# Kernel optimization log

Hardware: AMD Instinct MI355X
Metric: run time of the kernel (lower is better)

The kernel has to match this reference:

```python
import jax, jax.numpy as jnp
import numpy as np
import math

B, S, H, E, TOPK, NHEADS = 8, 512, 1024, 8, 2, 8
CAP = int(B * S * 1.5 * TOPK / E)  # 1536


def _linear(x, w, b):
    # torch nn.Linear convention: y = x @ w.T + b, w: [out, in]
    return x @ w.T + b


def _mha(x, in_w, in_b, out_w, out_b, n_heads):
    # torch nn.MultiheadAttention self-attention, eval mode (no dropout)
    Bx, Sx, D = x.shape
    dh = D // n_heads
    qkv = x @ in_w.T + in_b                      # [B,S,3D]
    q, k, v = jnp.split(qkv, 3, axis=-1)
    def heads(t):
        return t.reshape(Bx, Sx, n_heads, dh).transpose(0, 2, 1, 3)  # [B,h,S,dh]
    q, k, v = heads(q), heads(k), heads(v)
    scores = jnp.einsum('bhqd,bhkd->bhqk', q, k) / math.sqrt(dh)
    attn = jax.nn.softmax(scores, axis=-1)
    o = jnp.einsum('bhqk,bhkd->bhqd', attn, v)   # [B,h,S,dh]
    o = o.transpose(0, 2, 1, 3).reshape(Bx, Sx, D)
    return o @ out_w.T + out_b


def setup_inputs() -> dict:
    key = jax.random.key(0)
    ks = jax.random.split(key, 24)
    sc = 0.02
    d = {
        'hidden_states': jax.random.normal(ks[0], (B, S, H), jnp.float32),
        'pos_emb': jax.random.normal(ks[1], (S, H), jnp.float32) * sc,
        'se_w1': jax.random.normal(ks[2], (H // 4, 1), jnp.float32) * sc,
        'se_b1': jnp.zeros((H // 4,), jnp.float32),
        'se_w2': jax.random.normal(ks[3], (H // 4, H // 4), jnp.float32) * sc,
        'se_b2': jnp.zeros((H // 4,), jnp.float32),
        'sexp_w': jax.random.normal(ks[4], (H, H // 4), jnp.float32) * sc,
        'sexp_b': jnp.zeros((H,), jnp.float32),
        'te_w1': jax.random.normal(ks[5], (H, H + 2), jnp.float32) * sc,
        'te_b1': jnp.zeros((H,), jnp.float32),
        'te_w2': jax.random.normal(ks[6], (H, H), jnp.float32) * sc,
        'te_b2': jnp.zeros((H,), jnp.float32),
        'attn_in_w': jax.random.normal(ks[7], (3 * H, H), jnp.float32) * sc,
        'attn_in_b': jnp.zeros((3 * H,), jnp.float32),
        'attn_out_w': jax.random.normal(ks[8], (H, H), jnp.float32) * sc,
        'attn_out_b': jnp.zeros((H,), jnp.float32),
        'tr_w1': jax.random.normal(ks[9], (H, H), jnp.float32) * sc,
        'tr_b1': jnp.zeros((H,), jnp.float32),
        'tr_w2': jax.random.normal(ks[10], (E, H), jnp.float32) * sc,
        'tr_b2': jnp.zeros((E,), jnp.float32),
    }
    return d


def reference(hidden_states, pos_emb, se_w1, se_b1, se_w2, se_b2, sexp_w, sexp_b,
              te_w1, te_b1, te_w2, te_b2, attn_in_w, attn_in_b, attn_out_w, attn_out_b,
              tr_w1, tr_b1, tr_w2, tr_b2):
    b, s, h = hidden_states.shape
    timestamps = jnp.arange(s, dtype=hidden_states.dtype)           # [S]
    seasonality = jnp.sin(timestamps * 2 * jnp.pi / 24)             # [S]
    ts_b = jnp.broadcast_to(timestamps, (b, s))
    se_b = jnp.broadcast_to(seasonality, (b, s))

    position_embeddings = pos_emb[:s][None]                          # [1,S,H]
    seas = jax.nn.relu(_linear(se_b[..., None], se_w1, se_b1))       # [B,S,H/4]
    seas = _linear(seas, se_w2, se_b2)
    seasonal_embeddings = _linear(seas, sexp_w, sexp_b)              # [B,S,H]

    time_features = jnp.stack([ts_b, se_b], axis=-1)                 # [B,S,2]
    combined = jnp.concatenate([hidden_states, time_features], -1)   # [B,S,H+2]
    enc = jax.nn.relu(_linear(combined, te_w1, te_b1))
    enc = _linear(enc, te_w2, te_b2)
    enc = enc + position_embeddings + seasonal_embeddings
    enc = _mha(enc, attn_in_w, attn_in_b, attn_out_w, attn_out_b, NHEADS)

    logits = _linear(jax.nn.relu(_linear(enc, tr_w1, tr_b1)), tr_w2, tr_b2)  # [B,S,E]
    router_probs = jax.nn.softmax(logits, axis=-1)
    top_k_probs, top_k_idx = jax.lax.top_k(router_probs, TOPK)
    top_k_probs = top_k_probs / top_k_probs.sum(-1, keepdims=True)

    capacity = int(b * s * 1.5 * TOPK / E)
    # top-k indices are distinct per token, so summed one-hots replicate the
    # python loop's slot-0 writes exactly.
    onehot = jax.nn.one_hot(top_k_idx, E, dtype=router_probs.dtype)  # [B,S,K,E]
    disp0 = onehot.sum(axis=2)                                        # [B,S,E]
    comb0 = jnp.einsum('bske,bsk->bse', onehot, top_k_probs)          # [B,S,E]
    dispatch = jnp.zeros((b, s, E, capacity), router_probs.dtype).at[:, :, :, 0].set(disp0)
    combine = jnp.zeros((b, s, E, capacity), router_probs.dtype).at[:, :, :, 0].set(comb0)

    p_mean = router_probs.mean(axis=(0, 1))
    aux_loss = jnp.sum(p_mean * jnp.log(p_mean * E + 1e-9))
    return dispatch, combine, router_probs, aux_loss
```

## Files before the change

kernel.cpp:

```cpp
#include <hip/hip_runtime.h>
#include <hip/hip_bf16.h>


#define Hh 1024

typedef __attribute__((ext_vector_type(8))) short short8v;
typedef __attribute__((ext_vector_type(4))) float f32x4;

static __device__ __forceinline__ ushort f2bf(float x) {
  uint u = __float_as_uint(x);
  u += 0x7FFF + ((u >> 16) & 1);
  return (ushort)(u >> 16);
}
static __device__ __forceinline__ float bf2f(ushort h) {
  return __uint_as_float(((uint)h) << 16);
}

template<int EPI, bool RELU, bool HAS_BN, bool HAS_BSN>
__global__ __launch_bounds__(256) void mgemm_k(
    const ushort* __restrict__ A, int lda, long long sAmaj, long long sAmin, int aHi, int aLo,
    const ushort* __restrict__ B, int ldb, long long sBmaj, long long sBmin, int bHi, int bLo,
    float* __restrict__ Cf, ushort* __restrict__ Ch, int ldc, long long sCmaj, long long sCmin,
    int splitOff, int Kd, int zdiv,
    const float* __restrict__ bN, const float* __restrict__ bSN, int ldbs, int smod,
    float alpha)
{
  int gx = gridDim.x, gy = gridDim.y;
  int lin = (blockIdx.z * gy + blockIdx.y) * gx + blockIdx.x;
  int nwg = gx * gy * gridDim.z;
  int cpx = nwg >> 3;
  int swz = (lin & 7) * cpx + (lin >> 3);
  int bz = swz / (gx * gy);
  int rem = swz - bz * (gx * gy);
  int by = rem / gx, bx = rem - by * gx;

  int zj = bz / zdiv, zi = bz - zj * zdiv;
  A += (size_t)zj * sAmaj + (size_t)zi * sAmin;
  B += (size_t)zj * sBmaj + (size_t)zi * sBmin;
  long long coff = (long long)zj * sCmaj + (long long)zi * sCmin;

  int m0 = by * 128, n0 = bx * 128;

  __shared__ __align__(16) ushort smem[32768];

  int t = threadIdx.x;
  int l = t & 63, w = t >> 6;
  int wm = w >> 1, wn = w & 1;

  f32x4 acc[4][4];
#pragma unroll
  for (int i = 0; i < 4; ++i)
#pragma unroll
    for (int j = 0; j < 4; ++j) acc[i][j] = (f32x4){0.f, 0.f, 0.f, 0.f};

  int srow = t >> 1;
  int sc = (t & 1) * 2;
  const ushort* gAh = A + (size_t)(m0 + srow) * lda + aHi + sc * 8;
  const ushort* gAl = A + (size_t)(m0 + srow) * lda + aLo + sc * 8;
  const ushort* gBh = B + (size_t)(n0 + srow) * ldb + bHi + sc * 8;
  const ushort* gBl = B + (size_t)(n0 + srow) * ldb + bLo + sc * 8;
  int wsw = ((srow >> 1) & 7) << 4;
  int wo0 = (srow * 64 + sc * 16) ^ wsw;
  int wo1 = (srow * 64 + sc * 16 + 16) ^ wsw;

  int aoff[4], boff[4];
#pragma unroll
  for (int mi = 0; mi < 4; ++mi) {
    int row = wm * 64 + mi * 16 + (l & 15);
    aoff[mi] = (row * 64 + (l >> 4) * 16) ^ (((row >> 1) & 7) << 4);
  }
#pragma unroll
  for (int ni = 0; ni < 4; ++ni) {
    int row = wn * 64 + ni * 16 + (l & 15);
    boff[ni] = (row * 64 + (l >> 4) * 16) ^ (((row >> 1) & 7) << 4);
  }

  int4 rAh0, rAh1, rAl0, rAl1, rBh0, rBh1, rBl0, rBl1;
#define LOADK(kc) do { \
    rAh0 = *(const int4*)(gAh + (kc));  rAh1 = *(const int4*)(gAh + (kc) + 8); \
    rAl0 = *(const int4*)(gAl + (kc));  rAl1 = *(const int4*)(gAl + (kc) + 8); \
    rBh0 = *(const int4*)(gBh + (kc));  rBh1 = *(const int4*)(gBh + (kc) + 8); \
    rBl0 = *(const int4*)(gBl + (kc));  rBl1 = *(const int4*)(gBl + (kc) + 8); \
  } while (0)
#define STOREK(bufbase) do { \
    char* nb_ = (char*)smem + (bufbase); \
    *(int4*)(nb_ + wo0) = rAh0;          *(int4*)(nb_ + wo1) = rAh1; \
    *(int4*)(nb_ + 8192 + wo0) = rAl0;   *(int4*)(nb_ + 8192 + wo1) = rAl1; \
    *(int4*)(nb_ + 16384 + wo0) = rBh0;  *(int4*)(nb_ + 16384 + wo1) = rBh1; \
    *(int4*)(nb_ + 24576 + wo0) = rBl0;  *(int4*)(nb_ + 24576 + wo1) = rBl1; \
  } while (0)

  int nt = Kd >> 5;
  LOADK(0);
  STOREK(0);
  __syncthreads();
  int cur = 0;
  for (int s2 = 0; s2 < nt; ++s2) {
    bool more = (s2 + 1 < nt);
    if (more) LOADK((s2 + 1) * 32);
    char* base = (char*)smem + cur * 32768;
    short8v ah[4], al[4], bb[4];
#pragma unroll
    for (int mi = 0; mi < 4; ++mi) ah[mi] = *(const short8v*)(base + aoff[mi]);
#pragma unroll
    for (int mi = 0; mi < 4; ++mi) al[mi] = *(const short8v*)(base + 8192 + aoff[mi]);
#pragma unroll
    for (int ni = 0; ni < 4; ++ni) bb[ni] = *(const short8v*)(base + 16384 + boff[ni]);
#pragma unroll
    for (int mi = 0; mi < 4; ++mi)
#pragma unroll
      for (int ni = 0; ni < 4; ++ni)
        acc[mi][ni] = __builtin_amdgcn_mfma_f32_16x16x32_bf16(ah[mi], bb[ni], acc[mi][ni], 0, 0, 0);
#pragma unroll
    for (int mi = 0; mi < 4; ++mi)
#pragma unroll
      for (int ni = 0; ni < 4; ++ni)
        acc[mi][ni] = __builtin_amdgcn_mfma_f32_16x16x32_bf16(al[mi], bb[ni], acc[mi][ni], 0, 0, 0);
#pragma unroll
    for (int ni = 0; ni < 4; ++ni) bb[ni] = *(const short8v*)(base + 24576 + boff[ni]);
#pragma unroll
    for (int mi = 0; mi < 4; ++mi)
#pragma unroll
      for (int ni = 0; ni < 4; ++ni)
        acc[mi][ni] = __builtin_amdgcn_mfma_f32_16x16x32_bf16(ah[mi], bb[ni], acc[mi][ni], 0, 0, 0);
    if (more) STOREK((cur ^ 1) * 32768);
    __syncthreads();
    cur ^= 1;
  }
#undef LOADK
#undef STOREK

#pragma unroll
  for (int mi = 0; mi < 4; ++mi)
#pragma unroll
    for (int j = 0; j < 4; ++j) {
      int m = m0 + wm * 64 + mi * 16 + (l >> 4) * 4 + j;
#pragma unroll
      for (int ni = 0; ni < 4; ++ni) {
        int n = n0 + wn * 64 + ni * 16 + (l & 15);
        float x = acc[mi][ni][j] * alpha;
        if (HAS_BN) x += bN[n];
        if (HAS_BSN) x += bSN[(size_t)(m % smod) * ldbs + n];
        if (RELU) x = fmaxf(x, 0.f);
        acc[mi][ni][j] = x;
      }
    }

  if (EPI == 0) {
    float* Fs = (float*)smem;
#pragma unroll
    for (int p = 0; p < 2; ++p) {
      __syncthreads();
      if (wm == p) {
#pragma unroll
        for (int mi = 0; mi < 4; ++mi)
#pragma unroll
          for (int j = 0; j < 4; ++j) {
            int r = mi * 16 + (l >> 4) * 4 + j;
#pragma unroll
            for (int ni = 0; ni < 4; ++ni) {
              int c = wn * 64 + ni * 16 + (l & 15);
              *(float*)((char*)Fs + ((r * 512 + c * 4) ^ ((r & 7) << 4))) = acc[mi][ni][j];
            }
          }
      }
      __syncthreads();
#pragma unroll
      for (int r8 = 0; r8 < 8; ++r8) {
        int idx = r8 * 256 + t;
        int row = idx >> 5, slot = idx & 31;
        int4 v = *(const int4*)((char*)Fs + ((row * 512 + slot * 16) ^ ((row & 7) << 4)));
        *(int4*)(Cf + coff + (size_t)(m0 + p * 64 + row) * ldc + n0 + slot * 4) = v;
      }
    }
  } else {
    __syncthreads();
    ushort* Es = smem;
#pragma unroll
    for (int pass = 0; pass < 2; ++pass) {
#pragma unroll
      for (int mi = 0; mi < 4; ++mi)
#pragma unroll
        for (int j = 0; j < 4; ++j) {
          int lr = wm * 64 + mi * 16 + (l >> 4) * 4 + j;
#pragma unroll
          for (int ni = 0; ni < 4; ++ni) {
            int lcb = (wn * 64 + ni * 16 + (l & 15)) * 2;
            float x = acc[mi][ni][j];
            ushort h = f2bf(x);
            ushort vv = (pass == 0) ? h : f2bf(x - bf2f(h));
            *(ushort*)((char*)Es + ((lr * 256 + lcb) ^ ((lr & 7) << 4))) = vv;
          }
        }
      __syncthreads();
      int off = (pass == 0) ? 0 : splitOff;
#pragma unroll
      for (int r = 0; r < 8; ++r) {
        int idx = r * 256 + t;
        int row = idx >> 4, cb = (idx & 15) * 16;
        int4 v = *(const int4*)((char*)Es + ((row * 256 + cb) ^ ((row & 7) << 4)));
        *(int4*)((char*)(Ch + coff + (size_t)(m0 + row) * ldc + off + n0) + cb) = v;
      }
      if (pass == 0) __syncthreads();
    }
  }
}

__global__ __launch_bounds__(256) void vtrans_k(
    const ushort* __restrict__ qkv2, ushort* __restrict__ Vt)
{
  int kt = blockIdx.x;
  int bh = blockIdx.y;
  int b = bh >> 3, h = bh & 7;
  __shared__ ushort VT[16384];
  int t = threadIdx.x;
#pragma unroll
  for (int seg = 0; seg < 2; ++seg) {
    int csrc = 2048 + h * 128 + seg * 3072;
    if (seg) __syncthreads();
#pragma unroll
    for (int r = 0; r < 8; ++r) {
      int idx = r * 256 + t;
      int k = idx >> 4, ds = idx & 15;
      int4 v = *(const int4*)(qkv2 + (size_t)(b * 512 + kt * 128 + k) * 6144 + csrc + ds * 8);
      ushort tmp[8];
      *(int4*)tmp = v;
#pragma unroll
      for (int j = 0; j < 8; ++j) {
        int d = ds * 8 + j;
        VT[d * 128 + (k ^ ((d >> 3) << 3))] = tmp[j];
      }
    }
    __syncthreads();
#pragma unroll
    for (int r = 0; r < 8; ++r) {
      int idx = r * 256 + t;
      int d = idx >> 4, os = idx & 15;
      int slot = os ^ (d >> 3);
      int4 v = *(const int4*)(VT + d * 128 + slot * 8);
      *(int4*)(Vt + (size_t)bh * 131072 + (size_t)d * 1024 + seg * 512 + kt * 128 + os * 8) = v;
    }
  }
}

__global__ __launch_bounds__(256) void convert_k(
    const float* __restrict__ W, int lda, ushort* __restrict__ Whl, int K)
{
  int r = blockIdx.x;
  int c = threadIdx.x * 4;
  const float* src = W + (size_t)r * lda + c;
  float x0 = src[0], x1 = src[1], x2 = src[2], x3 = src[3];
  ushort4 h, lo;
  h.x = f2bf(x0); lo.x = f2bf(x0 - bf2f(h.x));
  h.y = f2bf(x1); lo.y = f2bf(x1 - bf2f(h.y));
  h.z = f2bf(x2); lo.z = f2bf(x2 - bf2f(h.z));
  h.w = f2bf(x3); lo.w = f2bf(x3 - bf2f(h.w));
  ushort* dst = Whl + (size_t)r * 2 * K;
  *(ushort4*)&dst[c] = h;
  *(ushort4*)&dst[K + c] = lo;
}

__global__ __launch_bounds__(256) void precompute_k(
    const float* __restrict__ pos_emb,
    const float* __restrict__ se_w1, const float* __restrict__ se_b1,
    const float* __restrict__ se_w2, const float* __restrict__ se_b2,
    const float* __restrict__ sexp_w, const float* __restrict__ sexp_b,
    const float* __restrict__ te_w1, const float* __restrict__ te_b1,
    float* __restrict__ psea, float* __restrict__ bias1)
{
  int s = blockIdx.x, t = threadIdx.x;
  float ts = (float)s;
  float se = sinf(((ts * 2.0f) * 3.14159274101257324f) / 24.0f);
  __shared__ float l1[256], l2[256];
  l1[t] = fmaxf(se * se_w1[t] + se_b1[t], 0.f);
  __syncthreads();
  {
    float a = se_b2[t];
    const float* wr = se_w2 + (size_t)t * 256;
    for (int i = 0; i < 256; ++i) a += l1[i] * wr[i];
    l2[t] = a;
  }
  __syncthreads();
#pragma unroll
  for (int r = 0; r < 4; ++r) {
    int h = r * 256 + t;
    float v = sexp_b[h];
    const float* wr = sexp_w + (size_t)h * 256;
    for (int j = 0; j < 256; ++j) v += l2[j] * wr[j];
    psea[s * Hh + h] = pos_emb[s * Hh + h] + v;
    bias1[s * Hh + h] = te_b1[h] + ts * te_w1[(size_t)h * 1026 + 1024]
                                 + se * te_w1[(size_t)h * 1026 + 1025];
  }
}

__global__ __launch_bounds__(256) void softmax2_k(float* __restrict__ S)
{
  int row = blockIdx.x * 4 + (threadIdx.x >> 6);
  int lane = threadIdx.x & 63;
  float* p = S + (size_t)row * 512;
  float4 a = *(float4*)&p[lane * 4];
  float4 b = *(float4*)&p[256 + lane * 4];
  float m = fmaxf(fmaxf(fmaxf(a.x, a.y), fmaxf(a.z, a.w)),
                  fmaxf(fmaxf(b.x, b.y), fmaxf(b.z, b.w)));
#pragma unroll
  for (int off = 32; off; off >>= 1) m = fmaxf(m, __shfl_xor(m, off));
  a.x = expf(a.x - m); a.y = expf(a.y - m); a.z = expf(a.z - m); a.w = expf(a.w - m);
  b.x = expf(b.x - m); b.y = expf(b.y - m); b.z = expf(b.z - m); b.w = expf(b.w - m);
  float s = a.x + a.y + a.z + a.w + b.x + b.y + b.z + b.w;
#pragma unroll
  for (int off = 32; off; off >>= 1) s += __shfl_xor(s, off);
  float inv = 1.f / s;
  a.x *= inv; a.y *= inv; a.z *= inv; a.w *= inv;
  b.x *= inv; b.y *= inv; b.z *= inv; b.w *= inv;
  ushort* u = (ushort*)S + (size_t)row * 1024;
  ushort4 ha, la, hb, lb;
  ha.x = f2bf(a.x); la.x = f2bf(a.x - bf2f(ha.x));
  ha.y = f2bf(a.y); la.y = f2bf(a.y - bf2f(ha.y));
  ha.z = f2bf(a.z); la.z = f2bf(a.z - bf2f(ha.z));
  ha.w = f2bf(a.w); la.w = f2bf(a.w - bf2f(ha.w));
  hb.x = f2bf(b.x); lb.x = f2bf(b.x - bf2f(hb.x));
  hb.y = f2bf(b.y); lb.y = f2bf(b.y - bf2f(hb.y));
  hb.z = f2bf(b.z); lb.z = f2bf(b.z - bf2f(hb.z));
  hb.w = f2bf(b.w); lb.w = f2bf(b.w - bf2f(hb.w));
  *(ushort4*)&u[lane * 4] = ha;
  *(ushort4*)&u[512 + lane * 4] = la;
  *(ushort4*)&u[256 + lane * 4] = hb;
  *(ushort4*)&u[768 + lane * 4] = lb;
}

__global__ __launch_bounds__(256) void tr2_k(
    const float* __restrict__ h1, const float* __restrict__ w,
    const float* __restrict__ bias, float* __restrict__ logits)
{
  int wid = threadIdx.x >> 6, lane = threadIdx.x & 63;
  int t = blockIdx.x * 4 + wid;
  const float* x = h1 + (size_t)t * Hh;
  float acc[8];
#pragma unroll
  for (int e = 0; e < 8; ++e) acc[e] = 0.f;
  for (int k = lane; k < Hh; k += 64) {
    float xv = x[k];
#pragma unroll
    for (int e = 0; e < 8; ++e) acc[e] += xv * w[e * Hh + k];
  }
#pragma unroll
  for (int e = 0; e < 8; ++e) {
#pragma unroll
    for (int off = 32; off; off >>= 1) acc[e] += __shfl_xor(acc[e], off);
  }
  if (lane == 0) {
#pragma unroll
    for (int e = 0; e < 8; ++e) logits[(size_t)t * 8 + e] = acc[e] + bias[e];
  }
}

__global__ __launch_bounds__(256) void fill0_k(float4* __restrict__ p, long long n4)
{
  long long i = (long long)blockIdx.x * 256 + threadIdx.x;
  long long stride = (long long)gridDim.x * 256;
  float4 z = make_float4(0.f, 0.f, 0.f, 0.f);
  for (; i < n4; i += stride) p[i] = z;
}

__global__ __launch_bounds__(256) void router_k(
    float* __restrict__ out, float* __restrict__ partials)
{
  int t = blockIdx.x * 256 + threadIdx.x;
  float* lg = out + 100663296 + (size_t)t * 8;
  float p[8];
#pragma unroll
  for (int e = 0; e < 8; ++e) p[e] = lg[e];
  float m = p[0];
#pragma unroll
  for (int e = 1; e < 8; ++e) m = fmaxf(m, p[e]);
  float s = 0.f;
#pragma unroll
  for (int e = 0; e < 8; ++e) { p[e] = expf(p[e] - m); s += p[e]; }
  float inv = 1.f / s;
#pragma unroll
  for (int e = 0; e < 8; ++e) p[e] *= inv;
#pragma unroll
  for (int e = 0; e < 8; ++e) lg[e] = p[e];

  int i0 = 0; float v0 = p[0];
#pragma unroll
  for (int e = 1; e < 8; ++e) if (p[e] > v0) { v0 = p[e]; i0 = e; }
  int i1 = -1; float v1 = -1.f;
#pragma unroll
  for (int e = 0; e < 8; ++e) if (e != i0 && p[e] > v1) { v1 = p[e]; i1 = e; }
  float wn = 1.f / (v0 + v1);
  size_t db = (size_t)t * (8 * 1536);
  out[db + (size_t)i0 * 1536] = 1.f;
  out[db + (size_t)i1 * 1536] = 1.f;
  out[50331648 + db + (size_t)i0 * 1536] = v0 * wn;
  out[50331648 + db + (size_t)i1 * 1536] = v1 * wn;

  __shared__ float red[256];
#pragma unroll
  for (int e = 0; e < 8; ++e) {
    red[threadIdx.x] = p[e];
    __syncthreads();
    for (int st = 128; st; st >>= 1) {
      if (threadIdx.x < st) red[threadIdx.x] += red[threadIdx.x + st];
      __syncthreads();
    }
    if (threadIdx.x == 0) partials[blockIdx.x * 8 + e] = red[0];
    __syncthreads();
  }
}

__global__ __launch_bounds__(64) void aux_k(float* __restrict__ partials,
                                            float* __restrict__ out)
{
  int lane = threadIdx.x;
  float v = 0.f;
  if (lane < 8) {
    float s = 0.f;
    for (int b = 0; b < 16; ++b) s += partials[b * 8 + lane];
    float pm = s / 4096.f;
    v = pm * logf(pm * 8.f + 1e-9f);
  }
#pragma unroll
  for (int off = 4; off; off >>= 1) v += __shfl_xor(v, off);
  if (lane == 0) out[100696064] = v;
  partials[lane] = 0.f;
  partials[64 + lane] = 0.f;
}

extern "C" void kernel_launch(void* const* d_in, const int* in_sizes, int n_in,
                              void* d_out, int out_size, void* d_ws, size_t ws_size,
                              hipStream_t stream)
{
  const float* hidden = (const float*)d_in[0];
  const float* pos_emb = (const float*)d_in[1];
  const float* se_w1 = (const float*)d_in[2];
  const float* se_b1 = (const float*)d_in[3];
  const float* se_w2 = (const float*)d_in[4];
  const float* se_b2 = (const float*)d_in[5];
  const float* sexp_w = (const float*)d_in[6];
  const float* sexp_b = (const float*)d_in[7];
  const float* te_w1 = (const float*)d_in[8];
  const float* te_b1 = (const float*)d_in[9];
  const float* te_w2 = (const float*)d_in[10];
  const float* te_b2 = (const float*)d_in[11];
  const float* ain_w = (const float*)d_in[12];
  const float* ain_b = (const float*)d_in[13];
  const float* aout_w = (const float*)d_in[14];
  const float* aout_b = (const float*)d_in[15];
  const float* tr_w1 = (const float*)d_in[16];
  const float* tr_b1 = (const float*)d_in[17];
  const float* tr_w2 = (const float*)d_in[18];
  const float* tr_b2 = (const float*)d_in[19];
  float* out = (float*)d_out;

  char* arena = (char*)d_out;
  ushort* W1    = (ushort*)(arena + 0);
  ushort* W2h   = (ushort*)(arena + 4194304);
  ushort* Wa    = (ushort*)(arena + 8388608);
  ushort* Wo    = (ushort*)(arena + 20971520);
  ushort* Wt    = (ushort*)(arena + 25165824);
  ushort* hid2  = (ushort*)(arena + 29360128);
  ushort* enc1  = (ushort*)(arena + 46137344);
  ushort* enc2  = (ushort*)(arena + 62914560);
  ushort* qkv2  = (ushort*)(arena + 79691776);
  float*  scor  = (float*)(arena + 130023424);
  ushort* attno = (ushort*)(arena + 197132288);
  ushort* encf  = (ushort*)(arena + 213909504);
  float*  h1    = (float*)(arena + 230686720);
  float*  psea  = (float*)(arena + 247463936);
  float*  bias1 = (float*)(arena + 249561088);
  ushort* Vt    = (ushort*)(arena + 251658240);
  float*  parts = out + 51380224;
  float*  lgts  = out + 100663296;

  convert_k<<<1024, 256, 0, stream>>>(te_w1, 1026, W1, 1024);
  convert_k<<<1024, 256, 0, stream>>>(te_w2, 1024, W2h, 1024);
  convert_k<<<3072, 256, 0, stream>>>(ain_w, 1024, Wa, 1024);
  convert_k<<<1024, 256, 0, stream>>>(aout_w, 1024, Wo, 1024);
  convert_k<<<1024, 256, 0, stream>>>(tr_w1, 1024, Wt, 1024);
  convert_k<<<4096, 256, 0, stream>>>(hidden, 1024, hid2, 1024);

  precompute_k<<<512, 256, 0, stream>>>(pos_emb, se_w1, se_b1, se_w2, se_b2,
                                        sexp_w, sexp_b, te_w1, te_b1, psea, bias1);

  mgemm_k<1, true, false, true><<<dim3(8, 32, 1), 256, 0, stream>>>(
      hid2, 2048, 0, 0, 0, 1024,
      W1, 2048, 0, 0, 0, 1024,
      nullptr, enc1, 2048, 0, 0, 1024,
      1024, 1, nullptr, bias1, 1024, 512, 1.f);

  mgemm_k<1, false, true, true><<<dim3(8, 32, 1), 256, 0, stream>>>(
      enc1, 2048, 0, 0, 0, 1024,
      W2h, 2048, 0, 0, 0, 1024,
      nullptr, enc2, 2048, 0, 0, 1024,
      1024, 1, te_b2, psea, 1024, 512, 1.f);

  mgemm_k<1, false, true, false><<<dim3(24, 32, 1), 256, 0, stream>>>(
      enc2, 2048, 0, 0, 0, 1024,
      Wa, 2048, 0, 0, 0, 1024,
      nullptr, qkv2, 6144, 0, 0, 3072,
      1024, 1, ain_b, nullptr, 1, 1, 1.f);

  mgemm_k<0, false, false, false><<<dim3(4, 4, 64), 256, 0, stream>>>(
      qkv2, 6144, 3145728, 128, 0, 3072,
      qkv2, 6144, 3145728, 128, 1024, 4096,
      scor, nullptr, 512, 2097152, 262144,
      0, 128, 8, nullptr, nullptr, 1, 1, 0.08838834764831845f);

  softmax2_k<<<8192, 256, 0, stream>>>(scor);

  vtrans_k<<<dim3(4, 64), 256, 0, stream>>>(qkv2, Vt);

  mgemm_k<1, false, false, false><<<dim3(1, 4, 64), 256, 0, stream>>>(
      (const ushort*)scor, 1024, 4194304, 524288, 0, 512,
      Vt, 1024, 1048576, 131072, 0, 512,
      nullptr, attno, 2048, 1048576, 128,
      1024, 512, 8, nullptr, nullptr, 1, 1, 1.f);

  mgemm_k<1, false, true, false><<<dim3(8, 32, 1), 256, 0, stream>>>(
      attno, 2048, 0, 0, 0, 1024,
      Wo, 2048, 0, 0, 0, 1024,
      nullptr, encf, 2048, 0, 0, 1024,
      1024, 1, aout_b, nullptr, 1, 1, 1.f);

  mgemm_k<0, true, true, false><<<dim3(8, 32, 1), 256, 0, stream>>>(
      encf, 2048, 0, 0, 0, 1024,
      Wt, 2048, 0, 0, 0, 1024,
      h1, nullptr, 1024, 0, 0, 0,
      1024, 1, tr_b1, nullptr, 1, 1, 1.f);

  tr2_k<<<1024, 256, 0, stream>>>(h1, tr_w2, tr_b2, lgts);

  fill0_k<<<4096, 256, 0, stream>>>((float4*)out, 25165824LL);

  router_k<<<16, 256, 0, stream>>>(out, parts);
  aux_k<<<1, 64, 0, stream>>>(parts, out);
}
```

Baseline: 527.6 us.

## Pre-swizzle B operands into MFMA fragment layout and load directly to registers

Weights and K/V are now stored pre-arranged in MFMA fragment order, split into hi and lo bf16 parts. The GEMM loads the B operand straight from global memory into registers, and only the A tiles go through LDS, which halves shared memory and allows two blocks per CU. The QKV GEMM epilogue writes K and V directly in fragment layout, with V transposed, so the separate V transpose kernel is removed. The cost is more register pressure from the double-buffered B fragments, and global loads of B are no longer shared between waves through LDS.

```diff
diff --git a/kernel.cpp b/kernel.cpp
--- a/kernel.cpp
+++ b/kernel.cpp
@@ -17,11 +17,13 @@
 }
 
 template<int EPI, bool RELU, bool HAS_BN, bool HAS_BSN>
-__global__ __launch_bounds__(256) void mgemm_k(
+__global__ __launch_bounds__(256, 2) void mgemm_k(
     const ushort* __restrict__ A, int lda, long long sAmaj, long long sAmin, int aHi, int aLo,
-    const ushort* __restrict__ B, int ldb, long long sBmaj, long long sBmin, int bHi, int bLo,
+    const ushort* __restrict__ Bf, int BNT, int BKC, long long sBmaj, long long sBmin,
     float* __restrict__ Cf, ushort* __restrict__ Ch, int ldc, long long sCmaj, long long sCmin,
-    int splitOff, int Kd, int zdiv,
+    int splitOff,
+    ushort* __restrict__ pK, ushort* __restrict__ pV,
+    int Kd, int zdiv,
     const float* __restrict__ bN, const float* __restrict__ bSN, int ldbs, int smod,
     float alpha)
 {
@@ -36,12 +38,12 @@
 
   int zj = bz / zdiv, zi = bz - zj * zdiv;
   A += (size_t)zj * sAmaj + (size_t)zi * sAmin;
-  B += (size_t)zj * sBmaj + (size_t)zi * sBmin;
+  const ushort* bfb = Bf + (size_t)zj * sBmaj + (size_t)zi * sBmin;
   long long coff = (long long)zj * sCmaj + (long long)zi * sCmin;
 
   int m0 = by * 128, n0 = bx * 128;
 
-  __shared__ __align__(16) ushort smem[32768];
+  __shared__ __align__(16) ushort smem[16384];
 
   int t = threadIdx.x;
   int l = t & 63, w = t >> 6;
@@ -57,78 +59,78 @@
   int sc = (t & 1) * 2;
   const ushort* gAh = A + (size_t)(m0 + srow) * lda + aHi + sc * 8;
   const ushort* gAl = A + (size_t)(m0 + srow) * lda + aLo + sc * 8;
-  const ushort* gBh = B + (size_t)(n0 + srow) * ldb + bHi + sc * 8;
-  const ushort* gBl = B + (size_t)(n0 + srow) * ldb + bLo + sc * 8;
   int wsw = ((srow >> 1) & 7) << 4;
   int wo0 = (srow * 64 + sc * 16) ^ wsw;
-  int wo1 = (srow * 64 + sc * 16 + 16) ^ wsw;
-
-  int aoff[4], boff[4];
+  int wo1 = wo0 ^ 16;
+
+  int aoff[4];
 #pragma unroll
   for (int mi = 0; mi < 4; ++mi) {
     int row = wm * 64 + mi * 16 + (l & 15);
     aoff[mi] = (row * 64 + (l >> 4) * 16) ^ (((row >> 1) & 7) << 4);
   }
+
+  const ushort* bph[4];
+  const ushort* bpl[4];
+  int ntg0 = (n0 >> 4) + wn * 4;
 #pragma unroll
   for (int ni = 0; ni < 4; ++ni) {
-    int row = wn * 64 + ni * 16 + (l & 15);
-    boff[ni] = (row * 64 + (l >> 4) * 16) ^ (((row >> 1) & 7) << 4);
-  }
-
-  int4 rAh0, rAh1, rAl0, rAl1, rBh0, rBh1, rBl0, rBl1;
-#define LOADK(kc) do { \
-    rAh0 = *(const int4*)(gAh + (kc));  rAh1 = *(const int4*)(gAh + (kc) + 8); \
-    rAl0 = *(const int4*)(gAl + (kc));  rAl1 = *(const int4*)(gAl + (kc) + 8); \
-    rBh0 = *(const int4*)(gBh + (kc));  rBh1 = *(const int4*)(gBh + (kc) + 8); \
-    rBl0 = *(const int4*)(gBl + (kc));  rBl1 = *(const int4*)(gBl + (kc) + 8); \
-  } while (0)
-#define STOREK(bufbase) do { \
-    char* nb_ = (char*)smem + (bufbase); \
-    *(int4*)(nb_ + wo0) = rAh0;          *(int4*)(nb_ + wo1) = rAh1; \
-    *(int4*)(nb_ + 8192 + wo0) = rAl0;   *(int4*)(nb_ + 8192 + wo1) = rAl1; \
-    *(int4*)(nb_ + 16384 + wo0) = rBh0;  *(int4*)(nb_ + 16384 + wo1) = rBh1; \
-    *(int4*)(nb_ + 24576 + wo0) = rBl0;  *(int4*)(nb_ + 24576 + wo1) = rBl1; \
-  } while (0)
+    bph[ni] = bfb + ((size_t)(ntg0 + ni) * BKC) * 512 + l * 8;
+    bpl[ni] = bfb + ((size_t)(BNT + ntg0 + ni) * BKC) * 512 + l * 8;
+  }
+
+  int4 a0h0, a0h1, a0l0, a0l1, a1h0, a1h1, a1l0, a1l1;
+  short8v B0h[4], B0l[4], B1h[4], B1l[4];
+
+#define LOADA0(s) { a0h0 = *(const int4*)(gAh + (s)*32); a0h1 = *(const int4*)(gAh + (s)*32 + 8); \
+                    a0l0 = *(const int4*)(gAl + (s)*32); a0l1 = *(const int4*)(gAl + (s)*32 + 8); }
+#define LOADA1(s) { a1h0 = *(const int4*)(gAh + (s)*32); a1h1 = *(const int4*)(gAh + (s)*32 + 8); \
+                    a1l0 = *(const int4*)(gAl + (s)*32); a1l1 = *(const int4*)(gAl + (s)*32 + 8); }
+#define STOREA(h0, h1, l0, l1, base) { char* nb = (char*)smem + (base); \
+    *(int4*)(nb + wo0) = h0; *(int4*)(nb + wo1) = h1; \
+    *(int4*)(nb + 8192 + wo0) = l0; *(int4*)(nb + 8192 + wo1) = l1; }
+#define LOADB(BH, BL, s) { _Pragma("unroll") \
+    for (int ni = 0; ni < 4; ++ni) { \
+      BH[ni] = *(const short8v*)(bph[ni] + (size_t)(s) * 512); \
+      BL[ni] = *(const short8v*)(bpl[ni] + (size_t)(s) * 512); } }
+#define MFMA_STEP(ahb, alb, BH, BL) { \
+    short8v ah[4], al[4]; \
+    _Pragma("unroll") for (int mi = 0; mi < 4; ++mi) \
+      ah[mi] = *(const short8v*)((char*)smem + (ahb) + aoff[mi]); \
+    _Pragma("unroll") for (int mi = 0; mi < 4; ++mi) \
+      al[mi] = *(const short8v*)((char*)smem + (alb) + aoff[mi]); \
+    _Pragma("unroll") for (int ni = 0; ni < 4; ++ni) \
+      _Pragma("unroll") for (int mi = 0; mi < 4; ++mi) \
+        acc[mi][ni] = __builtin_amdgcn_mfma_f32_16x16x32_bf16(ah[mi], BH[ni], acc[mi][ni], 0, 0, 0); \
+    _Pragma("unroll") for (int ni = 0; ni < 4; ++ni) \
+      _Pragma("unroll") for (int mi = 0; mi < 4; ++mi) \
+        acc[mi][ni] = __builtin_amdgcn_mfma_f32_16x16x32_bf16(al[mi], BH[ni], acc[mi][ni], 0, 0, 0); \
+    _Pragma("unroll") for (int ni = 0; ni < 4; ++ni) \
+      _Pragma("unroll") for (int mi = 0; mi < 4; ++mi) \
+        acc[mi][ni] = __builtin_amdgcn_mfma_f32_16x16x32_bf16(ah[mi], BL[ni], acc[mi][ni], 0, 0, 0); }
 
   int nt = Kd >> 5;
-  LOADK(0);
-  STOREK(0);
+  LOADA0(0); LOADB(B0h, B0l, 0);
+  LOADA1(1); LOADB(B1h, B1l, 1);
+  STOREA(a0h0, a0h1, a0l0, a0l1, 0);
   __syncthreads();
-  int cur = 0;
-  for (int s2 = 0; s2 < nt; ++s2) {
-    bool more = (s2 + 1 < nt);
-    if (more) LOADK((s2 + 1) * 32);
-    char* base = (char*)smem + cur * 32768;
-    short8v ah[4], al[4], bb[4];
-#pragma unroll
-    for (int mi = 0; mi < 4; ++mi) ah[mi] = *(const short8v*)(base + aoff[mi]);
-#pragma unroll
-    for (int mi = 0; mi < 4; ++mi) al[mi] = *(const short8v*)(base + 8192 + aoff[mi]);
-#pragma unroll
-    for (int ni = 0; ni < 4; ++ni) bb[ni] = *(const short8v*)(base + 16384 + boff[ni]);
-#pragma unroll
-    for (int mi = 0; mi < 4; ++mi)
-#pragma unroll
-      for (int ni = 0; ni < 4; ++ni)
-        acc[mi][ni] = __builtin_amdgcn_mfma_f32_16x16x32_bf16(ah[mi], bb[ni], acc[mi][ni], 0, 0, 0);
-#pragma unroll
-    for (int mi = 0; mi < 4; ++mi)
-#pragma unroll
-      for (int ni = 0; ni < 4; ++ni)
-        acc[mi][ni] = __builtin_amdgcn_mfma_f32_16x16x32_bf16(al[mi], bb[ni], acc[mi][ni], 0, 0, 0);
-#pragma unroll
-    for (int ni = 0; ni < 4; ++ni) bb[ni] = *(const short8v*)(base + 24576 + boff[ni]);
-#pragma unroll
-    for (int mi = 0; mi < 4; ++mi)
-#pragma unroll
-      for (int ni = 0; ni < 4; ++ni)
-        acc[mi][ni] = __builtin_amdgcn_mfma_f32_16x16x32_bf16(ah[mi], bb[ni], acc[mi][ni], 0, 0, 0);
-    if (more) STOREK((cur ^ 1) * 32768);
+  for (int s2 = 0; s2 < nt; s2 += 2) {
+    if (s2 + 2 < nt) LOADA0(s2 + 2);
+    MFMA_STEP(0, 8192, B0h, B0l);
+    if (s2 + 2 < nt) LOADB(B0h, B0l, s2 + 2);
+    STOREA(a1h0, a1h1, a1l0, a1l1, 16384);
     __syncthreads();
-    cur ^= 1;
-  }
-#undef LOADK
-#undef STOREK
+    if (s2 + 3 < nt) LOADA1(s2 + 3);
+    MFMA_STEP(16384, 24576, B1h, B1l);
+    if (s2 + 3 < nt) LOADB(B1h, B1l, s2 + 3);
+    if (s2 + 2 < nt) STOREA(a0h0, a0h1, a0l0, a0l1, 0);
+    __syncthreads();
+  }
+#undef LOADA0
+#undef LOADA1
+#undef STOREA
+#undef LOADB
+#undef MFMA_STEP
 
 #pragma unroll
   for (int mi = 0; mi < 4; ++mi)
@@ -176,71 +178,111 @@
   } else {
     __syncthreads();
     ushort* Es = smem;
+    bool isQ = (EPI == 1) || (n0 < 1024);
+    bool isK = (EPI == 2) && !isQ && (n0 < 2048);
+    int bb = m0 >> 9, s0 = m0 & 511;
+    int hh2 = isK ? ((n0 - 1024) >> 7) : ((n0 - 2048) >> 7);
+    size_t kvb = (size_t)(bb * 8 + hh2) * 131072;
 #pragma unroll
     for (int pass = 0; pass < 2; ++pass) {
-#pragma unroll
-      for (int mi = 0; mi < 4; ++mi)
-#pragma unroll
-        for (int j = 0; j < 4; ++j) {
-          int lr = wm * 64 + mi * 16 + (l >> 4) * 4 + j;
-#pragma unroll
-          for (int ni = 0; ni < 4; ++ni) {
-            int lcb = (wn * 64 + ni * 16 + (l & 15)) * 2;
-            float x = acc[mi][ni][j];
-            ushort h = f2bf(x);
-            ushort vv = (pass == 0) ? h : f2bf(x - bf2f(h));
-            *(ushort*)((char*)Es + ((lr * 256 + lcb) ^ ((lr & 7) << 4))) = vv;
+      if (isQ) {
+#pragma unroll
+        for (int mi = 0; mi < 4; ++mi)
+#pragma unroll
+          for (int j = 0; j < 4; ++j) {
+            int lr = wm * 64 + mi * 16 + (l >> 4) * 4 + j;
+#pragma unroll
+            for (int ni = 0; ni < 4; ++ni) {
+              int lcb = (wn * 64 + ni * 16 + (l & 15)) * 2;
+              float x = acc[mi][ni][j];
+              ushort h = f2bf(x);
+              ushort vv = (pass == 0) ? h : f2bf(x - bf2f(h));
+              *(ushort*)((char*)Es + ((lr * 256 + lcb) ^ ((lr & 7) << 4))) = vv;
+            }
           }
+      } else if (isK) {
+#pragma unroll
+        for (int mi = 0; mi < 4; ++mi)
+#pragma unroll
+          for (int j = 0; j < 4; ++j) {
+            int lr = wm * 64 + mi * 16 + (l >> 4) * 4 + j;
+#pragma unroll
+            for (int ni = 0; ni < 4; ++ni) {
+              int lcb = (wn * 64 + ni * 16 + (l & 15)) * 2;
+              float x = acc[mi][ni][j];
+              ushort h = f2bf(x);
+              ushort vv = (pass == 0) ? h : f2bf(x - bf2f(h));
+              *(ushort*)((char*)Es + ((lr * 256 + lcb) ^ ((lr & 7) << 4))) = vv;
+            }
+          }
+      } else {
+#pragma unroll
+        for (int mi = 0; mi < 4; ++mi)
+#pragma unroll
+          for (int j = 0; j < 4; ++j) {
+            int cc = (wm * 64 + mi * 16 + (l >> 4) * 4 + j) * 2;
+#pragma unroll
+            for (int ni = 0; ni < 4; ++ni) {
+              int rr = wn * 64 + ni * 16 + (l & 15);
+              float x = acc[mi][ni][j];
+              ushort h = f2bf(x);
+              ushort vv = (pass == 0) ? h : f2bf(x - bf2f(h));
+              *(ushort*)((char*)Es + ((rr * 256 + cc) ^ ((rr & 7) << 4))) = vv;
+            }
+          }
+      }
+      __syncthreads();
+      if (isQ) {
+        int off = (pass == 0) ? 0 : splitOff;
+#pragma unroll
+        for (int r = 0; r < 8; ++r) {
+          int idx = r * 256 + t;
+          int row = idx >> 4, cb = (idx & 15) * 16;
+          int4 v = *(const int4*)((char*)Es + ((row * 256 + cb) ^ ((row & 7) << 4)));
+          *(int4*)((char*)(Ch + coff + (size_t)(m0 + row) * ldc + off + n0) + cb) = v;
         }
-      __syncthreads();
-      int off = (pass == 0) ? 0 : splitOff;
-#pragma unroll
-      for (int r = 0; r < 8; ++r) {
-        int idx = r * 256 + t;
-        int row = idx >> 4, cb = (idx & 15) * 16;
-        int4 v = *(const int4*)((char*)Es + ((row * 256 + cb) ^ ((row & 7) << 4)));
-        *(int4*)((char*)(Ch + coff + (size_t)(m0 + row) * ldc + off + n0) + cb) = v;
+      } else if (isK) {
+#pragma unroll
+        for (int sw = 0; sw < 8; ++sw) {
+          int idx = sw * 256 + t;
+          int f = idx >> 6, l2 = idx & 63;
+          int st = f >> 2, dc = f & 3;
+          int row = st * 16 + (l2 & 15);
+          int colB = (dc * 32 + ((l2 >> 4) << 3)) * 2;
+          short8v v = *(const short8v*)((char*)Es + ((row * 256 + colB) ^ ((row & 7) << 4)));
+          *(short8v*)(pK + kvb + (size_t)((pass * 32 + (s0 >> 4) + st) * 4 + dc) * 512 + l2 * 8) = v;
+        }
+      } else {
+#pragma unroll
+        for (int sw = 0; sw < 8; ++sw) {
+          int idx = sw * 256 + t;
+          int f = idx >> 6, l2 = idx & 63;
+          int dt = f >> 2, sch = f & 3;
+          int row = dt * 16 + (l2 & 15);
+          int colB = (sch * 32 + ((l2 >> 4) << 3)) * 2;
+          short8v v = *(const short8v*)((char*)Es + ((row * 256 + colB) ^ ((row & 7) << 4)));
+          *(short8v*)(pV + kvb + (size_t)((pass * 8 + dt) * 16 + (s0 >> 5) + sch) * 512 + l2 * 8) = v;
+        }
       }
       if (pass == 0) __syncthreads();
     }
   }
 }
 
-__global__ __launch_bounds__(256) void vtrans_k(
-    const ushort* __restrict__ qkv2, ushort* __restrict__ Vt)
-{
-  int kt = blockIdx.x;
-  int bh = blockIdx.y;
-  int b = bh >> 3, h = bh & 7;
-  __shared__ ushort VT[16384];
-  int t = threadIdx.x;
-#pragma unroll
-  for (int seg = 0; seg < 2; ++seg) {
-    int csrc = 2048 + h * 128 + seg * 3072;
-    if (seg) __syncthreads();
-#pragma unroll
-    for (int r = 0; r < 8; ++r) {
-      int idx = r * 256 + t;
-      int k = idx >> 4, ds = idx & 15;
-      int4 v = *(const int4*)(qkv2 + (size_t)(b * 512 + kt * 128 + k) * 6144 + csrc + ds * 8);
-      ushort tmp[8];
-      *(int4*)tmp = v;
-#pragma unroll
-      for (int j = 0; j < 8; ++j) {
-        int d = ds * 8 + j;
-        VT[d * 128 + (k ^ ((d >> 3) << 3))] = tmp[j];
-      }
-    }
-    __syncthreads();
-#pragma unroll
-    for (int r = 0; r < 8; ++r) {
-      int idx = r * 256 + t;
-      int d = idx >> 4, os = idx & 15;
-      int slot = os ^ (d >> 3);
-      int4 v = *(const int4*)(VT + d * 128 + slot * 8);
-      *(int4*)(Vt + (size_t)bh * 131072 + (size_t)d * 1024 + seg * 512 + kt * 128 + os * 8) = v;
-    }
-  }
+__global__ __launch_bounds__(64) void convertf_k(
+    const float* __restrict__ W, int ldw, ushort* __restrict__ Wf, int NT, int KC)
+{
+  int kc = blockIdx.x, nt2 = blockIdx.y, l = threadIdx.x;
+  const float* src = W + (size_t)(nt2 * 16 + (l & 15)) * ldw + kc * 32 + ((l >> 4) << 3);
+  ushort h8[8], l8[8];
+#pragma unroll
+  for (int j = 0; j < 8; ++j) {
+    float x = src[j];
+    h8[j] = f2bf(x);
+    l8[j] = f2bf(x - bf2f(h8[j]));
+  }
+  *(int4*)(Wf + ((size_t)nt2 * KC + kc) * 512 + l * 8) = *(int4*)h8;
+  *(int4*)(Wf + ((size_t)(NT + nt2) * KC + kc) * 512 + l * 8) = *(int4*)l8;
 }
 
 __global__ __launch_bounds__(256) void convert_k(
@@ -454,30 +496,31 @@
   float* out = (float*)d_out;
 
   char* arena = (char*)d_out;
-  ushort* W1    = (ushort*)(arena + 0);
-  ushort* W2h   = (ushort*)(arena + 4194304);
-  ushort* Wa    = (ushort*)(arena + 8388608);
-  ushort* Wo    = (ushort*)(arena + 20971520);
-  ushort* Wt    = (ushort*)(arena + 25165824);
-  ushort* hid2  = (ushort*)(arena + 29360128);
-  ushort* enc1  = (ushort*)(arena + 46137344);
-  ushort* enc2  = (ushort*)(arena + 62914560);
-  ushort* qkv2  = (ushort*)(arena + 79691776);
-  float*  scor  = (float*)(arena + 130023424);
-  ushort* attno = (ushort*)(arena + 197132288);
-  ushort* encf  = (ushort*)(arena + 213909504);
-  float*  h1    = (float*)(arena + 230686720);
-  float*  psea  = (float*)(arena + 247463936);
-  float*  bias1 = (float*)(arena + 249561088);
-  ushort* Vt    = (ushort*)(arena + 251658240);
-  float*  parts = out + 51380224;
-  float*  lgts  = out + 100663296;
-
-  convert_k<<<1024, 256, 0, stream>>>(te_w1, 1026, W1, 1024);
-  convert_k<<<1024, 256, 0, stream>>>(te_w2, 1024, W2h, 1024);
-  convert_k<<<3072, 256, 0, stream>>>(ain_w, 1024, Wa, 1024);
-  convert_k<<<1024, 256, 0, stream>>>(aout_w, 1024, Wo, 1024);
-  convert_k<<<1024, 256, 0, stream>>>(tr_w1, 1024, Wt, 1024);
+  ushort* W1f  = (ushort*)(arena + 0);
+  ushort* W2f  = (ushort*)(arena + 4194304);
+  ushort* Waf  = (ushort*)(arena + 8388608);
+  ushort* Wof  = (ushort*)(arena + 20971520);
+  ushort* Wtf  = (ushort*)(arena + 25165824);
+  ushort* hid2 = (ushort*)(arena + 29360128);
+  ushort* enc1 = (ushort*)(arena + 46137344);
+  ushort* enc2 = (ushort*)(arena + 62914560);
+  ushort* qbuf = (ushort*)(arena + 79691776);
+  ushort* Kf   = (ushort*)(arena + 96468992);
+  ushort* Vf   = (ushort*)(arena + 113246208);
+  float*  scor = (float*)(arena + 130023424);
+  ushort* attno= (ushort*)(arena + 197132288);
+  ushort* encf = (ushort*)(arena + 213909504);
+  float*  h1   = (float*)(arena + 230686720);
+  float*  psea = (float*)(arena + 247463936);
+  float*  bias1= (float*)(arena + 249561088);
+  float*  parts= out + 51380224;
+  float*  lgts = out + 100663296;
+
+  convertf_k<<<dim3(32, 64), 64, 0, stream>>>(te_w1, 1026, W1f, 64, 32);
+  convertf_k<<<dim3(32, 64), 64, 0, stream>>>(te_w2, 1024, W2f, 64, 32);
+  convertf_k<<<dim3(32, 192), 64, 0, stream>>>(ain_w, 1024, Waf, 192, 32);
+  convertf_k<<<dim3(32, 64), 64, 0, stream>>>(aout_w, 1024, Wof, 64, 32);
+  convertf_k<<<dim3(32, 64), 64, 0, stream>>>(tr_w1, 1024, Wtf, 64, 32);
   convert_k<<<4096, 256, 0, stream>>>(hidden, 1024, hid2, 1024);
 
   precompute_k<<<512, 256, 0, stream>>>(pos_emb, se_w1, se_b1, se_w2, se_b2,
@@ -485,48 +528,46 @@
 
   mgemm_k<1, true, false, true><<<dim3(8, 32, 1), 256, 0, stream>>>(
       hid2, 2048, 0, 0, 0, 1024,
-      W1, 2048, 0, 0, 0, 1024,
-      nullptr, enc1, 2048, 0, 0, 1024,
+      W1f, 64, 32, 0, 0,
+      nullptr, enc1, 2048, 0, 0, 1024, nullptr, nullptr,
       1024, 1, nullptr, bias1, 1024, 512, 1.f);
 
   mgemm_k<1, false, true, true><<<dim3(8, 32, 1), 256, 0, stream>>>(
       enc1, 2048, 0, 0, 0, 1024,
-      W2h, 2048, 0, 0, 0, 1024,
-      nullptr, enc2, 2048, 0, 0, 1024,
+      W2f, 64, 32, 0, 0,
+      nullptr, enc2, 2048, 0, 0, 1024, nullptr, nullptr,
       1024, 1, te_b2, psea, 1024, 512, 1.f);
 
-  mgemm_k<1, false, true, false><<<dim3(24, 32, 1), 256, 0, stream>>>(
+  mgemm_k<2, false, true, false><<<dim3(24, 32, 1), 256, 0, stream>>>(
       enc2, 2048, 0, 0, 0, 1024,
-      Wa, 2048, 0, 0, 0, 1024,
-      nullptr, qkv2, 6144, 0, 0, 3072,
+      Waf, 192, 32, 0, 0,
+      nullptr, qbuf, 2048, 0, 0, 1024, Kf, Vf,
       1024, 1, ain_b, nullptr, 1, 1, 1.f);
 
   mgemm_k<0, false, false, false><<<dim3(4, 4, 64), 256, 0, stream>>>(
-      qkv2, 6144, 3145728, 128, 0, 3072,
-      qkv2, 6144, 3145728, 128, 1024, 4096,
-      scor, nullptr, 512, 2097152, 262144,
-      0, 128, 8, nullptr, nullptr, 1, 1, 0.08838834764831845f);
+      qbuf, 2048, 1048576, 128, 0, 1024,
+      Kf, 32, 4, 1048576, 131072,
+      scor, nullptr, 512, 2097152, 262144, 0, nullptr, nullptr,
+      128, 8, nullptr, nullptr, 1, 1, 0.08838834764831845f);
 
   softmax2_k<<<8192, 256, 0, stream>>>(scor);
-
-  vtrans_k<<<dim3(4, 64), 256, 0, stream>>>(qkv2, Vt);
 
   mgemm_k<1, false, false, false><<<dim3(1, 4, 64), 256, 0, stream>>>(
       (const ushort*)scor, 1024, 4194304, 524288, 0, 512,
-      Vt, 1024, 1048576, 131072, 0, 512,
-      nullptr, attno, 2048, 1048576, 128,
-      1024, 512, 8, nullptr, nullptr, 1, 1, 1.f);
+      Vf, 8, 16, 1048576, 131072,
+      nullptr, attno, 2048, 1048576, 128, 1024, nullptr, nullptr,
+      512, 8, nullptr, nullptr, 1, 1, 1.f);
 
   mgemm_k<1, false, true, false><<<dim3(8, 32, 1), 256, 0, stream>>>(
       attno, 2048, 0, 0, 0, 1024,
-      Wo, 2048, 0, 0, 0, 1024,
-      nullptr, encf, 2048, 0, 0, 1024,
+      Wof, 64, 32, 0, 0,
+      nullptr, encf, 2048, 0, 0, 1024, nullptr, nullptr,
       1024, 1, aout_b, nullptr, 1, 1, 1.f);
 
   mgemm_k<0, true, true, false><<<dim3(8, 32, 1), 256, 0, stream>>>(
       encf, 2048, 0, 0, 0, 1024,
-      Wt, 2048, 0, 0, 0, 1024,
-      h1, nullptr, 1024, 0, 0, 0,
+      Wtf, 64, 32, 0, 0,
+      h1, nullptr, 1024, 0, 0, 0, nullptr, nullptr,
       1024, 1, tr_b1, nullptr, 1, 1, 1.f);
 
   tr2_k<<<1024, 256, 0, stream>>>(h1, tr_w2, tr_b2, lgts);
```

New measurement: 481.4 us. -8.7%, faster.
